# Kernel optimization log

Measured on AMD Instinct MI355X. Metric: run time of the kernel, lower is better.

## Reference

```python
import jax, jax.numpy as jnp
import numpy as np

NUM_NODES = 50000
IN_CH = 64
OUT_CH = 64
NUM_EDGES = 800000


def setup_inputs() -> dict:
    key = jax.random.key(0)
    k1, k2, k3, k4 = jax.random.split(key, 4)
    x = jax.random.normal(k1, (NUM_NODES, IN_CH), dtype=jnp.float32)
    edge_index = jax.random.randint(k2, (2, NUM_EDGES), 0, NUM_NODES, dtype=jnp.int64)
    # Xavier-uniform linear weight [out, 2*in], zero bias (torch convention W @ x^T + b)
    fan_in, fan_out = 2 * IN_CH, OUT_CH
    limit = np.sqrt(6.0 / (fan_in + fan_out))
    W = jax.random.uniform(k3, (OUT_CH, 2 * IN_CH), minval=-limit, maxval=limit, dtype=jnp.float32)
    b = jnp.zeros((OUT_CH,), dtype=jnp.float32)
    return {"x": x, "edge_index": edge_index, "W": W, "b": b}


def reference(x, edge_index, W, b):
    num_nodes = x.shape[0]
    row, col = edge_index[0], edge_index[1]
    # mean aggregation: scatter-add of x[row] into destination col, divide by degree
    aggr = jax.ops.segment_sum(x[row], col, num_segments=num_nodes)  # [N, C]
    deg = jax.ops.segment_sum(jnp.ones_like(col, dtype=x.dtype), col, num_segments=num_nodes)
    aggr = aggr / jnp.clip(deg, 1.0, None)[:, None]
    out = jnp.concatenate([x, aggr], axis=-1)  # [N, 2C]
    return out @ W.T + b
```

## Files before the change

### kernel.cpp

```cpp
#include <hip/hip_runtime.h>
#include <hip/hip_fp8.h>

#define NN 50000
#define NC 64
#define NE 800000
#define NGRP 3125
#define CAP 62
#define CONV_BLK 3125
#define FILL_BLK 391
#define EPB 2048
#define NPART 196
#define QCAP 4608
#define TS 288

typedef __attribute__((ext_vector_type(8))) short bf16x8;
typedef __attribute__((ext_vector_type(4))) float f32x4;

__device__ __forceinline__ unsigned short f32_to_bf16_rne(float v) {
    unsigned u = __float_as_uint(v);
    u = (u + 0x7fffu + ((u >> 16) & 1u)) >> 16;
    return (unsigned short)u;
}
__device__ __forceinline__ unsigned pack_bf16x2(float lo, float hi) {
    return (unsigned)f32_to_bf16_rne(lo) | ((unsigned)f32_to_bf16_rne(hi) << 16);
}

__device__ __forceinline__ unsigned char f32_to_fp8(float v) {
    __hip_fp8_e4m3 t(v);
    return (unsigned char)t.__x;
}
__device__ __forceinline__ float fp8_to_f32(unsigned b) {
    __hip_fp8_e4m3 t;
    t.__x = (__hip_fp8_storage_t)b;
    return (float)t;
}

__global__ __launch_bounds__(256) void convert_partition_kernel(
        const float4* __restrict__ x4, ushort4* __restrict__ xh4,
        unsigned* __restrict__ xf8,
        const int4* __restrict__ row4, const int4* __restrict__ col4,
        int* __restrict__ qcnt, unsigned* __restrict__ queue) {
    int b = blockIdx.x;
    if (b >= FILL_BLK) {
        int i = (b - FILL_BLK) * 256 + threadIdx.x;
        float4 v = x4[i];
        ushort4 h;
        h.x = f32_to_bf16_rne(v.x); h.y = f32_to_bf16_rne(v.y);
        h.z = f32_to_bf16_rne(v.z); h.w = f32_to_bf16_rne(v.w);
        xh4[i] = h;
        unsigned q = (unsigned)f32_to_fp8(v.x)
                   | ((unsigned)f32_to_fp8(v.y) << 8)
                   | ((unsigned)f32_to_fp8(v.z) << 16)
                   | ((unsigned)f32_to_fp8(v.w) << 24);
        xf8[i] = q;
        return;
    }
    __shared__ int lcnt[NPART];
    __shared__ int lstart[NPART];
    __shared__ int sbase[NPART];
    __shared__ int s[256];
    __shared__ int stot;
    __shared__ unsigned staged[EPB];

    const int tid = threadIdx.x;
    for (int i = tid; i < NPART; i += 256) lcnt[i] = 0;
    __syncthreads();

    unsigned ent[8];
    int      rk[8];
    int      nv[2];
#pragma unroll
    for (int j = 0; j < 2; ++j) {
        int t = b * (EPB / 4) + j * 256 + tid;
        nv[j] = (t < NE / 4);
        if (nv[j]) {
            int4 r = row4[t];
            int4 c = col4[t];
            int p;
            p = c.x >> 8; ent[j*4+0] = ((unsigned)p << 24) | ((unsigned)(c.x & 255) << 16) | (unsigned)r.x;
            rk[j*4+0] = atomicAdd(&lcnt[p], 1);
            p = c.y >> 8; ent[j*4+1] = ((unsigned)p << 24) | ((unsigned)(c.y & 255) << 16) | (unsigned)r.y;
            rk[j*4+1] = atomicAdd(&lcnt[p], 1);
            p = c.z >> 8; ent[j*4+2] = ((unsigned)p << 24) | ((unsigned)(c.z & 255) << 16) | (unsigned)r.z;
            rk[j*4+2] = atomicAdd(&lcnt[p], 1);
            p = c.w >> 8; ent[j*4+3] = ((unsigned)p << 24) | ((unsigned)(c.w & 255) << 16) | (unsigned)r.w;
            rk[j*4+3] = atomicAdd(&lcnt[p], 1);
        }
    }
    __syncthreads();

    int v = (tid < NPART) ? lcnt[tid] : 0;
    s[tid] = v;
    __syncthreads();
#pragma unroll
    for (int d = 1; d < 256; d <<= 1) {
        int u = (tid >= d) ? s[tid - d] : 0;
        __syncthreads();
        s[tid] += u;
        __syncthreads();
    }
    if (tid < NPART) {
        lstart[tid] = s[tid] - v;
        sbase[tid]  = atomicAdd(&qcnt[tid], v);
    }
    if (tid == NPART - 1) stot = s[tid];
    __syncthreads();

#pragma unroll
    for (int j = 0; j < 2; ++j) {
        if (nv[j]) {
#pragma unroll
            for (int k = 0; k < 4; ++k) {
                unsigned e = ent[j*4+k];
                staged[lstart[e >> 24] + rk[j*4+k]] = e;
            }
        }
    }
    __syncthreads();

    int tot = stot;
    for (int i = tid; i < tot; i += 256) {
        unsigned e = staged[i];
        int p = (int)(e >> 24);
        int pos = sbase[p] + (i - lstart[p]);
        if (pos < QCAP) queue[p * QCAP + pos] = e;
    }
}

__global__ __launch_bounds__(256) void build_records_kernel(
        const int* __restrict__ qcnt, const unsigned* __restrict__ queue,
        uint4* __restrict__ rec4) {
    __shared__ __align__(16) char lrec[256 * 128];
    int p = blockIdx.x;
    uint4* lz = (uint4*)lrec;
    uint4 z; z.x = 0; z.y = 0; z.z = 0; z.w = 0;
#pragma unroll
    for (int i = 0; i < 8; ++i) lz[threadIdx.x + 256 * i] = z;
    __syncthreads();

    int qn = min(qcnt[p], QCAP);
    const unsigned* q = queue + p * QCAP;
    for (int i = threadIdx.x; i < qn; i += 256) {
        unsigned e = q[i];
        int n = (int)((e >> 16) & 255u);
        int pos = atomicAdd((int*)(lrec + n * 128), 1);
        if (pos < CAP)
            *(unsigned short*)(lrec + n * 128 + 4 + 2 * pos) =
                (unsigned short)(e & 0xffffu);
    }
    __syncthreads();

    uint4* dst = rec4 + (size_t)p * 2048;
#pragma unroll
    for (int i = 0; i < 8; ++i) dst[threadIdx.x + 256 * i] = lz[threadIdx.x + 256 * i];
}

__global__ __launch_bounds__(256) void gather_mfma_kernel(
        const uint4* __restrict__ xq,
        const uint2* __restrict__ xf,
        const int*   __restrict__ rec,
        const float* __restrict__ W,
        const float* __restrict__ b,
        float*       __restrict__ out) {
    __shared__ __align__(16) char tile[16 * TS];

    const int lane = threadIdx.x & 63;
    const int w    = threadIdx.x >> 6;
    const int g8   = lane >> 3;
    const int c8   = lane & 7;
    const int mg   = lane >> 4;
    const int mc   = lane & 15;

    bf16x8 bfrag[4];
    {
        const float* wr = W + (16 * w + mc) * 128;
#pragma unroll
        for (int ks = 0; ks < 4; ++ks) {
            int k0 = ks * 32 + mg * 8;
            float4 f0 = *(const float4*)(wr + k0);
            float4 f1 = *(const float4*)(wr + k0 + 4);
            bf16x8 f;
            f[0] = (short)f32_to_bf16_rne(f0.x); f[1] = (short)f32_to_bf16_rne(f0.y);
            f[2] = (short)f32_to_bf16_rne(f0.z); f[3] = (short)f32_to_bf16_rne(f0.w);
            f[4] = (short)f32_to_bf16_rne(f1.x); f[5] = (short)f32_to_bf16_rne(f1.y);
            f[6] = (short)f32_to_bf16_rne(f1.z); f[7] = (short)f32_to_bf16_rne(f1.w);
            bfrag[ks] = f;
        }
    }
    const float bv = b[16 * w + mc];
    const unsigned short* slots = (const unsigned short*)rec;

    {
        const int gi   = blockIdx.x;
        const int base = gi * 16;
        const int n0   = base + w * 4;

        int d0 = rec[(n0 + 0) << 5], d1 = rec[(n0 + 1) << 5],
            d2 = rec[(n0 + 2) << 5], d3 = rec[(n0 + 3) << 5];
        int l0 = min(d0, CAP), l1 = min(d1, CAP), l2 = min(d2, CAP), l3 = min(d3, CAP);
        int m  = max(max(l0, l1), max(l2, l3));
        int itn = (m + 7) >> 3;
        const int k0 = ((n0 + 0) << 6) + 2, k1 = ((n0 + 1) << 6) + 2,
                  k2 = ((n0 + 2) << 6) + 2, k3 = ((n0 + 3) << 6) + 2;

        float F0[8] = {0}, F1[8] = {0}, F2[8] = {0}, F3[8] = {0};
#define ACC8F8(F, wK, u) \
        F[0] = fmaf(wK, fp8_to_f32((u.x      ) & 0xffu), F[0]); \
        F[1] = fmaf(wK, fp8_to_f32((u.x >>  8) & 0xffu), F[1]); \
        F[2] = fmaf(wK, fp8_to_f32((u.x >> 16) & 0xffu), F[2]); \
        F[3] = fmaf(wK, fp8_to_f32((u.x >> 24)        ), F[3]); \
        F[4] = fmaf(wK, fp8_to_f32((u.y      ) & 0xffu), F[4]); \
        F[5] = fmaf(wK, fp8_to_f32((u.y >>  8) & 0xffu), F[5]); \
        F[6] = fmaf(wK, fp8_to_f32((u.y >> 16) & 0xffu), F[6]); \
        F[7] = fmaf(wK, fp8_to_f32((u.y >> 24)        ), F[7]);
        for (int it = 0, e = g8; it < itn; ++it, e += 8) {
            int b0 = (int)slots[k0 + e], b1 = (int)slots[k1 + e],
                b2 = (int)slots[k2 + e], b3 = (int)slots[k3 + e];
            int s0 = (e < l0) ? b0 : 0;
            int s1 = (e < l1) ? b1 : 0;
            int s2 = (e < l2) ? b2 : 0;
            int s3 = (e < l3) ? b3 : 0;
            float w0 = (e < l0) ? 1.f : 0.f;
            float w1 = (e < l1) ? 1.f : 0.f;
            float w2 = (e < l2) ? 1.f : 0.f;
            float w3 = (e < l3) ? 1.f : 0.f;
            uint2 u0 = xf[s0 * 8 + c8];
            uint2 u1 = xf[s1 * 8 + c8];
            uint2 u2 = xf[s2 * 8 + c8];
            uint2 u3 = xf[s3 * 8 + c8];
            ACC8F8(F0, w0, u0) ACC8F8(F1, w1, u1)
            ACC8F8(F2, w2, u2) ACC8F8(F3, w3, u3)
        }
#undef ACC8F8

#define RED8(F) \
        _Pragma("unroll") \
        for (int j = 0; j < 8; ++j) { \
            F[j] += __shfl_xor(F[j], 8, 64); \
            F[j] += __shfl_xor(F[j], 16, 64); \
            F[j] += __shfl_xor(F[j], 32, 64); \
        }
        RED8(F0) RED8(F1) RED8(F2) RED8(F3)
#undef RED8

        float inv0 = 1.0f / fmaxf((float)d0, 1.0f);
        float inv1 = 1.0f / fmaxf((float)d1, 1.0f);
        float inv2 = 1.0f / fmaxf((float)d2, 1.0f);
        float inv3 = 1.0f / fmaxf((float)d3, 1.0f);

        if (lane < 32) {
            int nk = lane >> 3, ch = lane & 7;
            uint4 sv = xq[(n0 + nk) * 8 + ch];
            *(uint4*)(tile + (w * 4 + nk) * TS + ch * 16) = sv;
        }
        if (lane < 8) {
            uint4 mv;
            mv.x = pack_bf16x2(F0[0] * inv0, F0[1] * inv0);
            mv.y = pack_bf16x2(F0[2] * inv0, F0[3] * inv0);
            mv.z = pack_bf16x2(F0[4] * inv0, F0[5] * inv0);
            mv.w = pack_bf16x2(F0[6] * inv0, F0[7] * inv0);
            *(uint4*)(tile + (w * 4 + 0) * TS + 128 + lane * 16) = mv;
            mv.x = pack_bf16x2(F1[0] * inv1, F1[1] * inv1);
            mv.y = pack_bf16x2(F1[2] * inv1, F1[3] * inv1);
            mv.z = pack_bf16x2(F1[4] * inv1, F1[5] * inv1);
            mv.w = pack_bf16x2(F1[6] * inv1, F1[7] * inv1);
            *(uint4*)(tile + (w * 4 + 1) * TS + 128 + lane * 16) = mv;
            mv.x = pack_bf16x2(F2[0] * inv2, F2[1] * inv2);
            mv.y = pack_bf16x2(F2[2] * inv2, F2[3] * inv2);
            mv.z = pack_bf16x2(F2[4] * inv2, F2[5] * inv2);
            mv.w = pack_bf16x2(F2[6] * inv2, F2[7] * inv2);
            *(uint4*)(tile + (w * 4 + 2) * TS + 128 + lane * 16) = mv;
            mv.x = pack_bf16x2(F3[0] * inv3, F3[1] * inv3);
            mv.y = pack_bf16x2(F3[2] * inv3, F3[3] * inv3);
            mv.z = pack_bf16x2(F3[4] * inv3, F3[5] * inv3);
            mv.w = pack_bf16x2(F3[6] * inv3, F3[7] * inv3);
            *(uint4*)(tile + (w * 4 + 3) * TS + 128 + lane * 16) = mv;
        }
        __syncthreads();

        f32x4 acc = {bv, bv, bv, bv};
#pragma unroll
        for (int ks = 0; ks < 4; ++ks) {
            bf16x8 af = *(const bf16x8*)(tile + mc * TS + ks * 64 + mg * 16);
            acc = __builtin_amdgcn_mfma_f32_16x16x32_bf16(af, bfrag[ks], acc, 0, 0, 0);
        }

#pragma unroll
        for (int r = 0; r < 4; ++r)
            out[(base + mg * 4 + r) * NC + 16 * w + mc] = acc[r];
    }
}

extern "C" void kernel_launch(void* const* d_in, const int* in_sizes, int n_in,
                              void* d_out, int out_size, void* d_ws, size_t ws_size,
                              hipStream_t stream) {
    const float* x   = (const float*)d_in[0];
    const int*   ei  = (const int*)d_in[1];
    const float* W   = (const float*)d_in[2];
    const float* b   = (const float*)d_in[3];
    float*       out = (float*)d_out;

    const int* row = ei;
    const int* col = ei + NE;

    int*      qcnt  = (int*)d_ws;
    unsigned* queue = (unsigned*)(qcnt + 256);
    int*      rec   = (int*)(queue + (size_t)NPART * QCAP);
    unsigned short* xh = (unsigned short*)(rec + (size_t)50176 * 32);
    unsigned* xf8 = (unsigned*)(xh + (size_t)NN * NC);

    hipMemsetAsync(qcnt, 0, 256 * sizeof(int), stream);

    convert_partition_kernel<<<FILL_BLK + CONV_BLK, 256, 0, stream>>>(
        (const float4*)x, (ushort4*)xh, xf8, (const int4*)row, (const int4*)col,
        qcnt, queue);

    build_records_kernel<<<NPART, 256, 0, stream>>>(
        qcnt, queue, (uint4*)rec);

    gather_mfma_kernel<<<NGRP, 256, 0, stream>>>(
        (const uint4*)xh, (const uint2*)xf8, rec, W, b, out);
}
```

Before: 124.1 us.

## Precompute bf16 weights, use wave-shuffle scan, padded LDS records, unroll gather loop

Adds one extra block to the convert kernel that converts W to bf16 once. The gather kernel then loads prepacked fragments after the gather loop instead of converting per block. The partition scan moves from a barrier-heavy LDS Hillis-Steele loop to a wave-level shuffle scan. build_records now uses a padded slot layout to cut LDS bank conflicts, and the gather loop is unrolled by two to put more loads in flight. The trade-offs are more registers in the gather and an extra workspace buffer.

```diff
diff --git a/kernel.cpp b/kernel.cpp
--- a/kernel.cpp
+++ b/kernel.cpp
@@ -39,8 +39,21 @@
         const float4* __restrict__ x4, ushort4* __restrict__ xh4,
         unsigned* __restrict__ xf8,
         const int4* __restrict__ row4, const int4* __restrict__ col4,
-        int* __restrict__ qcnt, unsigned* __restrict__ queue) {
+        int* __restrict__ qcnt, unsigned* __restrict__ queue,
+        const float4* __restrict__ W4, ushort4* __restrict__ wb4) {
     int b = blockIdx.x;
+    if (b >= FILL_BLK + CONV_BLK) {
+#pragma unroll
+        for (int j = 0; j < 8; ++j) {
+            int i = threadIdx.x + 256 * j;
+            float4 v = W4[i];
+            ushort4 h;
+            h.x = f32_to_bf16_rne(v.x); h.y = f32_to_bf16_rne(v.y);
+            h.z = f32_to_bf16_rne(v.z); h.w = f32_to_bf16_rne(v.w);
+            wb4[i] = h;
+        }
+        return;
+    }
     if (b >= FILL_BLK) {
         int i = (b - FILL_BLK) * 256 + threadIdx.x;
         float4 v = x4[i];
@@ -58,7 +71,7 @@
     __shared__ int lcnt[NPART];
     __shared__ int lstart[NPART];
     __shared__ int sbase[NPART];
-    __shared__ int s[256];
+    __shared__ int wpart[4];
     __shared__ int stot;
     __shared__ unsigned staged[EPB];
 
@@ -90,20 +103,28 @@
     __syncthreads();
 
     int v = (tid < NPART) ? lcnt[tid] : 0;
-    s[tid] = v;
-    __syncthreads();
-#pragma unroll
-    for (int d = 1; d < 256; d <<= 1) {
-        int u = (tid >= d) ? s[tid - d] : 0;
-        __syncthreads();
-        s[tid] += u;
-        __syncthreads();
-    }
-    if (tid < NPART) {
-        lstart[tid] = s[tid] - v;
-        sbase[tid]  = atomicAdd(&qcnt[tid], v);
-    }
-    if (tid == NPART - 1) stot = s[tid];
+    int sc = v;
+    const int lane2 = tid & 63;
+#pragma unroll
+    for (int d = 1; d < 64; d <<= 1) {
+        int u = __shfl_up(sc, (unsigned)d, 64);
+        if (lane2 >= d) sc += u;
+    }
+    if (lane2 == 63) wpart[tid >> 6] = sc;
+    __syncthreads();
+    {
+        int wid2 = tid >> 6;
+        int add = 0;
+        if (wid2 > 0) add += wpart[0];
+        if (wid2 > 1) add += wpart[1];
+        if (wid2 > 2) add += wpart[2];
+        int incl = sc + add;
+        if (tid < NPART) {
+            lstart[tid] = incl - v;
+            sbase[tid]  = atomicAdd(&qcnt[tid], v);
+        }
+        if (tid == 255) stot = incl;
+    }
     __syncthreads();
 
 #pragma unroll
@@ -130,36 +151,52 @@
 __global__ __launch_bounds__(256) void build_records_kernel(
         const int* __restrict__ qcnt, const unsigned* __restrict__ queue,
         uint4* __restrict__ rec4) {
-    __shared__ __align__(16) char lrec[256 * 128];
-    int p = blockIdx.x;
-    uint4* lz = (uint4*)lrec;
-    uint4 z; z.x = 0; z.y = 0; z.z = 0; z.w = 0;
-#pragma unroll
-    for (int i = 0; i < 8; ++i) lz[threadIdx.x + 256 * i] = z;
+    __shared__ __align__(16) unsigned short lslot[256 * 66];
+    __shared__ int lcnt[256];
+    const int p = blockIdx.x;
+    const int tid = threadIdx.x;
+    lcnt[tid] = 0;
     __syncthreads();
 
     int qn = min(qcnt[p], QCAP);
     const unsigned* q = queue + p * QCAP;
-    for (int i = threadIdx.x; i < qn; i += 256) {
+    for (int i = tid; i < qn; i += 256) {
         unsigned e = q[i];
         int n = (int)((e >> 16) & 255u);
-        int pos = atomicAdd((int*)(lrec + n * 128), 1);
+        int pos = atomicAdd(&lcnt[n], 1);
         if (pos < CAP)
-            *(unsigned short*)(lrec + n * 128 + 4 + 2 * pos) =
-                (unsigned short)(e & 0xffffu);
-    }
-    __syncthreads();
-
+            lslot[n * 66 + pos] = (unsigned short)(e & 0xffffu);
+    }
+    __syncthreads();
+
+    const unsigned* ls = (const unsigned*)lslot;
     uint4* dst = rec4 + (size_t)p * 2048;
 #pragma unroll
-    for (int i = 0; i < 8; ++i) dst[threadIdx.x + 256 * i] = lz[threadIdx.x + 256 * i];
+    for (int it = 0; it < 8; ++it) {
+        int i = tid + 256 * it;
+        int n = i >> 3, c = i & 7;
+        int base = n * 33 + 4 * c - 1;
+        uint4 g;
+        if (c == 0) {
+            g.x = (unsigned)lcnt[n];
+            g.y = ls[n * 33 + 0];
+            g.z = ls[n * 33 + 1];
+            g.w = ls[n * 33 + 2];
+        } else {
+            g.x = ls[base];
+            g.y = ls[base + 1];
+            g.z = ls[base + 2];
+            g.w = ls[base + 3];
+        }
+        dst[i] = g;
+    }
 }
 
 __global__ __launch_bounds__(256) void gather_mfma_kernel(
         const uint4* __restrict__ xq,
         const uint2* __restrict__ xf,
         const int*   __restrict__ rec,
-        const float* __restrict__ W,
+        const uint4* __restrict__ Wq,
         const float* __restrict__ b,
         float*       __restrict__ out) {
     __shared__ __align__(16) char tile[16 * TS];
@@ -171,22 +208,6 @@
     const int mg   = lane >> 4;
     const int mc   = lane & 15;
 
-    bf16x8 bfrag[4];
-    {
-        const float* wr = W + (16 * w + mc) * 128;
-#pragma unroll
-        for (int ks = 0; ks < 4; ++ks) {
-            int k0 = ks * 32 + mg * 8;
-            float4 f0 = *(const float4*)(wr + k0);
-            float4 f1 = *(const float4*)(wr + k0 + 4);
-            bf16x8 f;
-            f[0] = (short)f32_to_bf16_rne(f0.x); f[1] = (short)f32_to_bf16_rne(f0.y);
-            f[2] = (short)f32_to_bf16_rne(f0.z); f[3] = (short)f32_to_bf16_rne(f0.w);
-            f[4] = (short)f32_to_bf16_rne(f1.x); f[5] = (short)f32_to_bf16_rne(f1.y);
-            f[6] = (short)f32_to_bf16_rne(f1.z); f[7] = (short)f32_to_bf16_rne(f1.w);
-            bfrag[ks] = f;
-        }
-    }
     const float bv = b[16 * w + mc];
     const unsigned short* slots = (const unsigned short*)rec;
 
@@ -213,25 +234,42 @@
         F[5] = fmaf(wK, fp8_to_f32((u.y >>  8) & 0xffu), F[5]); \
         F[6] = fmaf(wK, fp8_to_f32((u.y >> 16) & 0xffu), F[6]); \
         F[7] = fmaf(wK, fp8_to_f32((u.y >> 24)        ), F[7]);
-        for (int it = 0, e = g8; it < itn; ++it, e += 8) {
-            int b0 = (int)slots[k0 + e], b1 = (int)slots[k1 + e],
-                b2 = (int)slots[k2 + e], b3 = (int)slots[k3 + e];
-            int s0 = (e < l0) ? b0 : 0;
-            int s1 = (e < l1) ? b1 : 0;
-            int s2 = (e < l2) ? b2 : 0;
-            int s3 = (e < l3) ? b3 : 0;
-            float w0 = (e < l0) ? 1.f : 0.f;
-            float w1 = (e < l1) ? 1.f : 0.f;
-            float w2 = (e < l2) ? 1.f : 0.f;
-            float w3 = (e < l3) ? 1.f : 0.f;
-            uint2 u0 = xf[s0 * 8 + c8];
-            uint2 u1 = xf[s1 * 8 + c8];
-            uint2 u2 = xf[s2 * 8 + c8];
-            uint2 u3 = xf[s3 * 8 + c8];
-            ACC8F8(F0, w0, u0) ACC8F8(F1, w1, u1)
-            ACC8F8(F2, w2, u2) ACC8F8(F3, w3, u3)
+        for (int it = 0, e = g8; it < itn; it += 2, e += 16) {
+            int eb = e + 8;
+            int a0 = (int)slots[k0 + e],  a1 = (int)slots[k1 + e],
+                a2 = (int)slots[k2 + e],  a3 = (int)slots[k3 + e];
+            int b0 = (int)slots[k0 + eb], b1 = (int)slots[k1 + eb],
+                b2 = (int)slots[k2 + eb], b3 = (int)slots[k3 + eb];
+            int sa0 = (e  < l0) ? a0 : 0;  float ma0 = (e  < l0) ? 1.f : 0.f;
+            int sa1 = (e  < l1) ? a1 : 0;  float ma1 = (e  < l1) ? 1.f : 0.f;
+            int sa2 = (e  < l2) ? a2 : 0;  float ma2 = (e  < l2) ? 1.f : 0.f;
+            int sa3 = (e  < l3) ? a3 : 0;  float ma3 = (e  < l3) ? 1.f : 0.f;
+            int sb0 = (eb < l0) ? b0 : 0;  float mb0 = (eb < l0) ? 1.f : 0.f;
+            int sb1 = (eb < l1) ? b1 : 0;  float mb1 = (eb < l1) ? 1.f : 0.f;
+            int sb2 = (eb < l2) ? b2 : 0;  float mb2 = (eb < l2) ? 1.f : 0.f;
+            int sb3 = (eb < l3) ? b3 : 0;  float mb3 = (eb < l3) ? 1.f : 0.f;
+            uint2 ua0 = xf[sa0 * 8 + c8];
+            uint2 ua1 = xf[sa1 * 8 + c8];
+            uint2 ua2 = xf[sa2 * 8 + c8];
+            uint2 ua3 = xf[sa3 * 8 + c8];
+            uint2 ub0 = xf[sb0 * 8 + c8];
+            uint2 ub1 = xf[sb1 * 8 + c8];
+            uint2 ub2 = xf[sb2 * 8 + c8];
+            uint2 ub3 = xf[sb3 * 8 + c8];
+            ACC8F8(F0, ma0, ua0) ACC8F8(F0, mb0, ub0)
+            ACC8F8(F1, ma1, ua1) ACC8F8(F1, mb1, ub1)
+            ACC8F8(F2, ma2, ua2) ACC8F8(F2, mb2, ub2)
+            ACC8F8(F3, ma3, ua3) ACC8F8(F3, mb3, ub3)
         }
 #undef ACC8F8
+
+        bf16x8 bfrag[4];
+        {
+            const uint4* wr = Wq + ((16 * w + mc) * 16 + mg);
+#pragma unroll
+            for (int ks = 0; ks < 4; ++ks)
+                bfrag[ks] = *(const bf16x8*)(wr + ks * 4);
+        }
 
 #define RED8(F) \
         _Pragma("unroll") \
@@ -308,16 +346,17 @@
     int*      rec   = (int*)(queue + (size_t)NPART * QCAP);
     unsigned short* xh = (unsigned short*)(rec + (size_t)50176 * 32);
     unsigned* xf8 = (unsigned*)(xh + (size_t)NN * NC);
+    unsigned short* wb = (unsigned short*)(xf8 + (size_t)NN * NC / 4);
 
     hipMemsetAsync(qcnt, 0, 256 * sizeof(int), stream);
 
-    convert_partition_kernel<<<FILL_BLK + CONV_BLK, 256, 0, stream>>>(
+    convert_partition_kernel<<<FILL_BLK + CONV_BLK + 1, 256, 0, stream>>>(
         (const float4*)x, (ushort4*)xh, xf8, (const int4*)row, (const int4*)col,
-        qcnt, queue);
+        qcnt, queue, (const float4*)W, (ushort4*)wb);
 
     build_records_kernel<<<NPART, 256, 0, stream>>>(
         qcnt, queue, (uint4*)rec);
 
     gather_mfma_kernel<<<NGRP, 256, 0, stream>>>(
-        (const uint4*)xh, (const uint2*)xf8, rec, W, b, out);
-}
+        (const uint4*)xh, (const uint2*)xf8, rec, (const uint4*)wb, b, out);
+}
```

Measured after the change: 115.9 us. 6.6% less time.
